# Performance work log

Hardware: AMD Instinct MI355X
Metric: run time of the kernel (lower is better)

The kernel has to match this reference:

```python
import jax, jax.numpy as jnp
import numpy as np
from jax import lax

B, D, H, W = 16, 256, 64, 64
P = 8  # patchsize
EPS = 1e-5


def setup_inputs() -> dict:
    key = jax.random.key(0)
    ks = jax.random.split(key, 8)
    s = 0.02
    return {
        "x": jax.random.normal(ks[0], (B, D, H, W), jnp.float32),
        "wq": jax.random.normal(ks[1], (D, D), jnp.float32) * s,
        "bq": jnp.zeros((D,), jnp.float32),
        "wk": jax.random.normal(ks[2], (D, D), jnp.float32) * s,
        "bk": jnp.zeros((D,), jnp.float32),
        "wv": jax.random.normal(ks[3], (D, D), jnp.float32) * s,
        "bv": jnp.zeros((D,), jnp.float32),
        "w_out": jax.random.normal(ks[4], (D, D, 3, 3), jnp.float32) * s,
        "b_out": jnp.zeros((D,), jnp.float32),
        "gamma": jnp.ones((D,), jnp.float32),
        "beta": jnp.zeros((D,), jnp.float32),
        "bn_mean": jnp.zeros((D,), jnp.float32),
        "bn_var": jnp.ones((D,), jnp.float32),
    }


def _conv1x1(x, w, b):
    # x: [b,c,h,w], w: [o,c] (1x1 conv) -> [b,o,h,w]
    return jnp.einsum('bchw,oc->bohw', x, w) + b[None, :, None, None]


def _to_patches(t, p):
    # [b,d,h,w] -> [b, p*p, d*hh*ww]  (matches view+permute(0,2,4,1,3,5)+view)
    b, d, h, w = t.shape
    hh, ww = h // p, w // p
    t = t.reshape(b, d, p, hh, p, ww).transpose(0, 2, 4, 1, 3, 5)
    return t.reshape(b, p * p, d * hh * ww)


def reference(x, wq, bq, wk, bk, wv, bv, w_out, b_out, gamma, beta, bn_mean, bn_var):
    b, d, h, w = x.shape
    p = P
    hh, ww = h // p, w // p

    q = _to_patches(_conv1x1(x, wq, bq), p)  # [b, p^2, d*hh*ww]
    k = _to_patches(_conv1x1(x, wk, bk), p)
    v = _to_patches(_conv1x1(x, wv, bv), p)

    scale = 1.0 / jnp.sqrt(jnp.asarray(q.shape[-1], q.dtype))
    scores = jnp.einsum('bqe,bke->bqk', q, k) * scale  # [b, p^2, p^2]
    attn = jax.nn.softmax(scores, axis=-1)
    out = jnp.einsum('bqk,bke->bqe', attn, v)  # [b, p^2, d*hh*ww]

    # [b,p,p,d,hh,ww] -> permute(0,3,1,4,2,5) -> [b,d,h,w]
    out = out.reshape(b, p, p, d, hh, ww).transpose(0, 3, 1, 4, 2, 5).reshape(b, d, h, w)

    # 3x3 conv, padding 1
    y = lax.conv_general_dilated(out, w_out, window_strides=(1, 1),
                                 padding=((1, 1), (1, 1)),
                                 dimension_numbers=('NCHW', 'OIHW', 'NCHW'))
    y = y + b_out[None, :, None, None]

    # BatchNorm2d (eval mode with running stats)
    inv = gamma / jnp.sqrt(bn_var + EPS)
    y = (y - bn_mean[None, :, None, None]) * inv[None, :, None, None] + beta[None, :, None, None]

    # LeakyReLU(0.2)
    return jnp.where(y >= 0, y, 0.2 * y)
```

## Files before the change

### kernel.cpp

```cpp
#include <hip/hip_runtime.h>
#include <hip/hip_bf16.h>

#define BB 16
#define SS 4096

typedef __attribute__((ext_vector_type(8))) short short8;
typedef __attribute__((ext_vector_type(4))) float float4v;

__global__ __launch_bounds__(256) void wprep_qkv(
    const float* __restrict__ wq, const float* __restrict__ wk,
    const float* __restrict__ wv, __hip_bfloat16* __restrict__ blob) {
  int chunk = blockIdx.x * 256 + threadIdx.x;
  int lane = chunk & 63;
  int ob = (chunk >> 6) & 15;
  int cb = (chunk >> 10) & 7;
  int which = chunk >> 13;
  const float* W = (which == 0) ? wq : (which == 1) ? wk : wv;
  int o = ob * 16 + (lane & 15);
  int c0 = cb * 32 + (lane >> 4) * 8;
  const float* p = W + o * 256 + c0;
  union { uint4 u; __hip_bfloat16 h[8]; } t;
#pragma unroll
  for (int j = 0; j < 8; ++j) t.h[j] = __float2bfloat16(p[j]);
  *reinterpret_cast<uint4*>(blob + (size_t)chunk * 8) = t.u;
}

__global__ __launch_bounds__(256) void qkv_mfma(
    const float* __restrict__ x, const __hip_bfloat16* __restrict__ blob,
    const float* __restrict__ bq, const float* __restrict__ bk,
    const float* __restrict__ bv,
    __hip_bfloat16* __restrict__ qb, __hip_bfloat16* __restrict__ kb,
    __hip_bfloat16* __restrict__ vb) {
  __shared__ short ls[64 * 40];
  const int which = blockIdx.z;
  const int b = blockIdx.y;
  const int s0 = blockIdx.x * 64;
  const float* bias = (which == 0) ? bq : (which == 1) ? bk : bv;
  __hip_bfloat16* outb = (which == 0) ? qb : kb;
  const int tid = threadIdx.x;
  const int wave = tid >> 6, lane = tid & 63;
  const int q = lane >> 4, m = lane & 15;
  const int sl = tid & 63;
  const int cg = tid >> 6;
  float4v acc[4][4] = {};

  for (int cb = 0; cb < 8; ++cb) {
    __syncthreads();
    {
      const float* xp = x + ((size_t)(b * 256 + cb * 32 + cg * 8)) * SS + s0 + sl;
      union { uint4 u; __hip_bfloat16 h[8]; } t;
#pragma unroll
      for (int i = 0; i < 8; ++i)
        t.h[i] = __float2bfloat16(xp[(size_t)i * SS]);
      *reinterpret_cast<uint4*>(&ls[sl * 40 + cg * 8]) = t.u;
    }
    __syncthreads();
    short8 af[4];
#pragma unroll
    for (int of = 0; of < 4; ++of)
      af[of] = *reinterpret_cast<const short8*>(
          blob +
          ((size_t)(((which * 8 + cb) * 16 + wave * 4 + of) * 64 + lane)) * 8);
    short8 xf[4];
#pragma unroll
    for (int sf = 0; sf < 4; ++sf)
      xf[sf] = *reinterpret_cast<const short8*>(&ls[(sf * 16 + m) * 40 + q * 8]);
#pragma unroll
    for (int of = 0; of < 4; ++of)
#pragma unroll
      for (int sf = 0; sf < 4; ++sf)
        acc[of][sf] = __builtin_amdgcn_mfma_f32_16x16x32_bf16(
            af[of], xf[sf], acc[of][sf], 0, 0, 0);
  }
  if (which == 2) {
    const int h = s0 >> 6;
#pragma unroll
    for (int of = 0; of < 4; ++of) {
      int o_base = wave * 64 + of * 16 + q * 4;
#pragma unroll
      for (int sf = 0; sf < 4; ++sf) {
        int w = sf * 16 + m;
        union { uint2 u; __hip_bfloat16 hh[4]; } t;
#pragma unroll
        for (int r = 0; r < 4; ++r)
          t.hh[r] = __float2bfloat16(acc[of][sf][r] + bias[o_base + r]);
        *reinterpret_cast<uint2*>(
            vb + ((size_t)((b * 64 + h) * 64 + w)) * 256 + o_base) = t.u;
      }
    }
  } else {
#pragma unroll
    for (int of = 0; of < 4; ++of) {
      int o_base = wave * 64 + of * 16 + q * 4;
#pragma unroll
      for (int r = 0; r < 4; ++r) {
        int o = o_base + r;
        float bi = bias[o];
        __hip_bfloat16* op = outb + ((size_t)(b * 256 + o)) * SS + s0 + m;
#pragma unroll
        for (int sf = 0; sf < 4; ++sf)
          op[sf * 16] = __float2bfloat16(acc[of][sf][r] + bi);
      }
    }
  }
}

__global__ __launch_bounds__(256) void scores_mfma(
    const __hip_bfloat16* __restrict__ qb, const __hip_bfloat16* __restrict__ kb,
    float* __restrict__ part) {
  const int b = blockIdx.y;
  const int d0 = blockIdx.x * 16;
  const int tid = threadIdx.x;
  const int wave = tid >> 6, lane = tid & 63;
  const int q = lane >> 4, m = lane & 15;
  const int t = wave * 16 + m;
  const int arow = (t >> 3) * 8;
  const int acol = (t & 7) * 8;
  float4v acc[4] = {};

  for (int dd = 0; dd < 16; ++dd) {
    const int d = d0 + dd;
    const __hip_bfloat16* qp = qb + ((size_t)(b * 256 + d)) * SS;
    const __hip_bfloat16* kp = kb + ((size_t)(b * 256 + d)) * SS;
#pragma unroll
    for (int khalf = 0; khalf < 2; ++khalf) {
      const int oh = khalf * 4 + q;
      short8 af = *reinterpret_cast<const short8*>(
          qp + (arow + oh) * 64 + acol);
      short8 bf[4];
#pragma unroll
      for (int nt = 0; nt < 4; ++nt) {
        int tp = nt * 16 + m;
        bf[nt] = *reinterpret_cast<const short8*>(
            kp + ((tp >> 3) * 8 + oh) * 64 + (tp & 7) * 8);
      }
#pragma unroll
      for (int nt = 0; nt < 4; ++nt)
        acc[nt] = __builtin_amdgcn_mfma_f32_16x16x32_bf16(af, bf[nt], acc[nt],
                                                          0, 0, 0);
    }
  }
  float* pp = part + ((size_t)(blockIdx.x * BB + b)) * 4096;
#pragma unroll
  for (int nt = 0; nt < 4; ++nt)
#pragma unroll
    for (int r = 0; r < 4; ++r)
      pp[(wave * 16 + q * 4 + r) * 64 + nt * 16 + m] = acc[nt][r];
}

__global__ __launch_bounds__(64) void softmax_kernel(
    const float* __restrict__ part, __hip_bfloat16* __restrict__ attnb) {
  const int t = blockIdx.x;
  const int b = blockIdx.y;
  const int lane = threadIdx.x;
  float v = 0.f;
#pragma unroll
  for (int sl = 0; sl < 16; ++sl)
    v += part[((size_t)(sl * BB + b)) * 4096 + t * 64 + lane];
  v *= 0.0078125f;
  float m = v;
#pragma unroll
  for (int off = 32; off >= 1; off >>= 1) m = fmaxf(m, __shfl_xor(m, off));
  float e = __expf(v - m);
  float s = e;
#pragma unroll
  for (int off = 32; off >= 1; off >>= 1) s += __shfl_xor(s, off);
  attnb[(b * 64 + t) * 64 + lane] = __float2bfloat16(e / s);
}

__global__ __launch_bounds__(256) void apply_mfma(
    const __hip_bfloat16* __restrict__ attnb, const __hip_bfloat16* __restrict__ vb,
    __hip_bfloat16* __restrict__ zb) {
  __shared__ short Vs[64][268];
  const int off = blockIdx.x;
  const int b = blockIdx.y;
  const int oh = off >> 3, ow = off & 7;
  const int tid = threadIdx.x;
#pragma unroll
  for (int i = 0; i < 8; ++i) {
    int chunk = i * 256 + tid;
    int tp = chunk >> 5;
    int cg = chunk & 31;
    int hh = (tp >> 3) * 8 + oh;
    int wwp = (tp & 7) * 8 + ow;
    uint4 val = *reinterpret_cast<const uint4*>(
        vb + ((size_t)((b * 64 + hh) * 64 + wwp)) * 256 + cg * 8);
    *reinterpret_cast<uint4*>(&Vs[tp][cg * 8]) = val;
  }
  __syncthreads();
  const int wave = tid >> 6, lane = tid & 63;
  const int q = lane >> 4, m = lane & 15;
  float4v acc[4][4] = {};
#pragma unroll
  for (int ks = 0; ks < 2; ++ks) {
    short8 af[4];
#pragma unroll
    for (int mt = 0; mt < 4; ++mt)
      af[mt] = *reinterpret_cast<const short8*>(
          attnb + (b * 64 + mt * 16 + m) * 64 + ks * 32 + q * 8);
    short8 bf[4];
#pragma unroll
    for (int nt = 0; nt < 4; ++nt) {
      int d = wave * 64 + nt * 16 + m;
      union { short8 v; short s[8]; } t;
#pragma unroll
      for (int j = 0; j < 8; ++j) t.s[j] = Vs[ks * 32 + q * 8 + j][d];
      bf[nt] = t.v;
    }
#pragma unroll
    for (int mt = 0; mt < 4; ++mt)
#pragma unroll
      for (int nt = 0; nt < 4; ++nt)
        acc[mt][nt] = __builtin_amdgcn_mfma_f32_16x16x32_bf16(
            af[mt], bf[nt], acc[mt][nt], 0, 0, 0);
  }
#pragma unroll
  for (int mt = 0; mt < 4; ++mt)
#pragma unroll
    for (int r = 0; r < 4; ++r) {
      int t = mt * 16 + q * 4 + r;
      int h = (t >> 3) * 8 + oh;
      int w = (t & 7) * 8 + ow;
      __hip_bfloat16* base = zb + ((size_t)((b * 64 + h) * 64 + w)) * 256;
#pragma unroll
      for (int nt = 0; nt < 4; ++nt)
        base[wave * 64 + nt * 16 + m] = __float2bfloat16(acc[mt][nt][r]);
    }
}

__global__ __launch_bounds__(256) void wprep(
    const float* __restrict__ wo, __hip_bfloat16* __restrict__ blob) {
  int chunk = blockIdx.x * 256 + threadIdx.x;
  int l = chunk & 63;
  int ob = (chunk >> 6) & 15;
  int cb = (chunk >> 10) & 7;
  int tap = chunk >> 13;
  int o = ob * 16 + (l & 15);
  int c0 = cb * 32 + (l >> 4) * 8;
  union { uint4 u; __hip_bfloat16 h[8]; } t;
#pragma unroll
  for (int j = 0; j < 8; ++j)
    t.h[j] = __float2bfloat16(wo[((size_t)(o * 256 + c0 + j)) * 9 + tap]);
  *reinterpret_cast<uint4*>(blob + (size_t)chunk * 8) = t.u;
}

__global__ __launch_bounds__(256) void conv_mfma(
    const __hip_bfloat16* __restrict__ z, const __hip_bfloat16* __restrict__ blob,
    const float* __restrict__ bo, const float* __restrict__ gm,
    const float* __restrict__ bt, const float* __restrict__ mn,
    const float* __restrict__ vr, float* __restrict__ out) {
  __shared__ short zs[2][3 * 66 * 42];
  const int idx0 = blockIdx.x;
  const int h = (idx0 & 7) * 8 + ((idx0 >> 3) & 7);
  const int b = idx0 >> 6;
  const int tid = threadIdx.x;
  const int wave = tid >> 6, lane = tid & 63;
  const int q = lane >> 4, m = lane & 15;
  float4v acc[4][4] = {};

  int s_r[4], s_wp[4], s_cg[4];
  bool s_ok[4];
  const __hip_bfloat16* s_base[4];
#pragma unroll
  for (int k = 0; k < 4; ++k) {
    int idx = tid + k * 256;
    bool act = idx < 792;
    int cg = idx & 3;
    int t2 = idx >> 2;
    int wpos = act ? (t2 % 66) : 0;
    int r = act ? (t2 / 66) : 0;
    int h_in = h - 1 + r;
    int w_in = wpos - 1;
    bool ok = act && h_in >= 0 && h_in < 64 && w_in >= 0 && w_in < 64;
    s_r[k] = r; s_wp[k] = wpos; s_cg[k] = cg; s_ok[k] = ok && act;
    s_ok[k] = ok;
    s_base[k] = z + ((size_t)((b * 64 + h_in) * 64 + w_in)) * 256 + cg * 8;
    if (!act) s_ok[k] = false;
    if (idx >= 792) { s_r[k] = 0; s_wp[k] = 0; s_cg[k] = 0; }
  }
  bool s_act[4];
#pragma unroll
  for (int k = 0; k < 4; ++k) s_act[k] = (tid + k * 256) < 792;

  uint4 pf[4];
#pragma unroll
  for (int k = 0; k < 4; ++k)
    pf[k] = s_ok[k] ? *reinterpret_cast<const uint4*>(s_base[k])
                    : make_uint4(0u, 0u, 0u, 0u);
#pragma unroll
  for (int k = 0; k < 4; ++k)
    if (s_act[k])
      *reinterpret_cast<uint4*>(
          &zs[0][(s_r[k] * 66 + s_wp[k]) * 42 + s_cg[k] * 8]) = pf[k];
  __syncthreads();

  for (int cb = 0; cb < 8; ++cb) {
    const short* cur = zs[cb & 1];
    short* nxt = zs[(cb + 1) & 1];
    if (cb < 7) {
#pragma unroll
      for (int k = 0; k < 4; ++k)
        pf[k] = s_ok[k] ? *reinterpret_cast<const uint4*>(
                              s_base[k] + (size_t)(cb + 1) * 32)
                        : make_uint4(0u, 0u, 0u, 0u);
    }
    for (int tap = 0; tap < 9; ++tap) {
      const int kh = tap / 3, kw = tap % 3;
      short8 wf[4];
#pragma unroll
      for (int of = 0; of < 4; ++of) {
        int ob = wave * 4 + of;
        wf[of] = *reinterpret_cast<const short8*>(
            blob + ((size_t)(((tap * 8 + cb) * 16 + ob) * 64 + lane)) * 8);
      }
      short8 zf[4];
#pragma unroll
      for (int wfi = 0; wfi < 4; ++wfi) {
        int wpos = wfi * 16 + m + kw;
        zf[wfi] = *reinterpret_cast<const short8*>(
            &cur[(kh * 66 + wpos) * 42 + q * 8]);
      }
#pragma unroll
      for (int of = 0; of < 4; ++of)
#pragma unroll
        for (int wfi = 0; wfi < 4; ++wfi)
          acc[of][wfi] = __builtin_amdgcn_mfma_f32_16x16x32_bf16(
              wf[of], zf[wfi], acc[of][wfi], 0, 0, 0);
    }
    if (cb < 7) {
#pragma unroll
      for (int k = 0; k < 4; ++k)
        if (s_act[k])
          *reinterpret_cast<uint4*>(
              &nxt[(s_r[k] * 66 + s_wp[k]) * 42 + s_cg[k] * 8]) = pf[k];
    }
    __syncthreads();
  }
#pragma unroll
  for (int of = 0; of < 4; ++of) {
    int o_base = wave * 64 + of * 16 + q * 4;
#pragma unroll
    for (int r = 0; r < 4; ++r) {
      int o = o_base + r;
      float sc = gm[o] * rsqrtf(vr[o] + 1e-5f);
      float sh = bt[o] + (bo[o] - mn[o]) * sc;
#pragma unroll
      for (int wfi = 0; wfi < 4; ++wfi) {
        float y = acc[of][wfi][r] * sc + sh;
        y = (y >= 0.f) ? y : 0.2f * y;
        out[(((size_t)(b * 256 + o)) * 64 + h) * 64 + wfi * 16 + m] = y;
      }
    }
  }
}

extern "C" void kernel_launch(void* const* d_in, const int* in_sizes, int n_in,
                              void* d_out, int out_size, void* d_ws,
                              size_t ws_size, hipStream_t stream) {
  (void)in_sizes; (void)n_in; (void)out_size; (void)ws_size;
  const float* x  = (const float*)d_in[0];
  const float* wq = (const float*)d_in[1];
  const float* bq = (const float*)d_in[2];
  const float* wk = (const float*)d_in[3];
  const float* bk = (const float*)d_in[4];
  const float* wv = (const float*)d_in[5];
  const float* bv = (const float*)d_in[6];
  const float* wo = (const float*)d_in[7];
  const float* bo = (const float*)d_in[8];
  const float* gm = (const float*)d_in[9];
  const float* bt = (const float*)d_in[10];
  const float* mn = (const float*)d_in[11];
  const float* vr = (const float*)d_in[12];
  float* out = (float*)d_out;

  char* ws = (char*)d_ws;
  __hip_bfloat16* qb = (__hip_bfloat16*)(ws);
  __hip_bfloat16* kb = (__hip_bfloat16*)(ws + 33554432);
  __hip_bfloat16* attnb = (__hip_bfloat16*)(ws + 67371008);
  __hip_bfloat16* blob = (__hip_bfloat16*)(ws + 67502080);
  __hip_bfloat16* vb = (__hip_bfloat16*)d_out;
  __hip_bfloat16* blob_a = (__hip_bfloat16*)((char*)d_out + 33554432);
  float* part = (float*)((char*)d_out + 37748736);

  wprep<<<288, 256, 0, stream>>>(wo, blob);
  wprep_qkv<<<96, 256, 0, stream>>>(wq, wk, wv, blob_a);
  qkv_mfma<<<dim3(64, BB, 3), 256, 0, stream>>>(x, blob_a, bq, bk, bv,
                                                qb, kb, vb);
  scores_mfma<<<dim3(16, BB), 256, 0, stream>>>(qb, kb, part);
  softmax_kernel<<<dim3(64, BB), 64, 0, stream>>>(part, attnb);
  apply_mfma<<<dim3(64, BB), 256, 0, stream>>>(attnb, vb, qb );
  conv_mfma<<<dim3(BB * 64), 256, 0, stream>>>(qb, blob, bo, gm, bt, mn, vr,
                                               out);
}
```

Measured before the change: 371.3 us.

## Fuse Q/K/V projections per block and prefetch conv weights in registers

The QKV projection now loads and converts the whole x tile (all 256 channels) into shared memory once per block and computes Q, K and V from it. Before, each of the three projections ran as its own grid slice and re-read x from global memory. The conv kernel double-buffers the weight fragments in registers, loading the next tap's weights while the current tap's MFMAs run. It also changes the shared-memory row pitch from 42 to 40 shorts and unrolls the tap loop. The trade-off is a larger shared-memory footprint and a third as many blocks in the QKV kernel, plus higher register pressure in conv, which may reduce occupancy and bring back LDS bank conflicts.

```diff
diff --git a/kernel.cpp b/kernel.cpp
--- a/kernel.cpp
+++ b/kernel.cpp
@@ -31,75 +31,78 @@
     const float* __restrict__ bv,
     __hip_bfloat16* __restrict__ qb, __hip_bfloat16* __restrict__ kb,
     __hip_bfloat16* __restrict__ vb) {
-  __shared__ short ls[64 * 40];
-  const int which = blockIdx.z;
+  __shared__ short ls[8][64 * 40];
   const int b = blockIdx.y;
   const int s0 = blockIdx.x * 64;
-  const float* bias = (which == 0) ? bq : (which == 1) ? bk : bv;
-  __hip_bfloat16* outb = (which == 0) ? qb : kb;
   const int tid = threadIdx.x;
   const int wave = tid >> 6, lane = tid & 63;
   const int q = lane >> 4, m = lane & 15;
   const int sl = tid & 63;
   const int cg = tid >> 6;
-  float4v acc[4][4] = {};
 
   for (int cb = 0; cb < 8; ++cb) {
-    __syncthreads();
-    {
-      const float* xp = x + ((size_t)(b * 256 + cb * 32 + cg * 8)) * SS + s0 + sl;
-      union { uint4 u; __hip_bfloat16 h[8]; } t;
-#pragma unroll
-      for (int i = 0; i < 8; ++i)
-        t.h[i] = __float2bfloat16(xp[(size_t)i * SS]);
-      *reinterpret_cast<uint4*>(&ls[sl * 40 + cg * 8]) = t.u;
-    }
-    __syncthreads();
-    short8 af[4];
-#pragma unroll
-    for (int of = 0; of < 4; ++of)
-      af[of] = *reinterpret_cast<const short8*>(
-          blob +
-          ((size_t)(((which * 8 + cb) * 16 + wave * 4 + of) * 64 + lane)) * 8);
-    short8 xf[4];
-#pragma unroll
-    for (int sf = 0; sf < 4; ++sf)
-      xf[sf] = *reinterpret_cast<const short8*>(&ls[(sf * 16 + m) * 40 + q * 8]);
-#pragma unroll
-    for (int of = 0; of < 4; ++of)
+    const float* xp = x + ((size_t)(b * 256 + cb * 32 + cg * 8)) * SS + s0 + sl;
+    union { uint4 u; __hip_bfloat16 h[8]; } t;
+#pragma unroll
+    for (int i = 0; i < 8; ++i)
+      t.h[i] = __float2bfloat16(xp[(size_t)i * SS]);
+    *reinterpret_cast<uint4*>(&ls[cb][sl * 40 + cg * 8]) = t.u;
+  }
+  __syncthreads();
+
+  for (int which = 0; which < 3; ++which) {
+    const float* bias = (which == 0) ? bq : (which == 1) ? bk : bv;
+    float4v acc[4][4] = {};
+#pragma unroll
+    for (int cb = 0; cb < 8; ++cb) {
+      short8 af[4];
+#pragma unroll
+      for (int of = 0; of < 4; ++of)
+        af[of] = *reinterpret_cast<const short8*>(
+            blob +
+            ((size_t)(((which * 8 + cb) * 16 + wave * 4 + of) * 64 + lane)) * 8);
+      short8 xf[4];
 #pragma unroll
       for (int sf = 0; sf < 4; ++sf)
-        acc[of][sf] = __builtin_amdgcn_mfma_f32_16x16x32_bf16(
-            af[of], xf[sf], acc[of][sf], 0, 0, 0);
-  }
-  if (which == 2) {
-    const int h = s0 >> 6;
-#pragma unroll
-    for (int of = 0; of < 4; ++of) {
-      int o_base = wave * 64 + of * 16 + q * 4;
-#pragma unroll
-      for (int sf = 0; sf < 4; ++sf) {
-        int w = sf * 16 + m;
-        union { uint2 u; __hip_bfloat16 hh[4]; } t;
-#pragma unroll
-        for (int r = 0; r < 4; ++r)
-          t.hh[r] = __float2bfloat16(acc[of][sf][r] + bias[o_base + r]);
-        *reinterpret_cast<uint2*>(
-            vb + ((size_t)((b * 64 + h) * 64 + w)) * 256 + o_base) = t.u;
-      }
-    }
-  } else {
-#pragma unroll
-    for (int of = 0; of < 4; ++of) {
-      int o_base = wave * 64 + of * 16 + q * 4;
-#pragma unroll
-      for (int r = 0; r < 4; ++r) {
-        int o = o_base + r;
-        float bi = bias[o];
-        __hip_bfloat16* op = outb + ((size_t)(b * 256 + o)) * SS + s0 + m;
+        xf[sf] =
+            *reinterpret_cast<const short8*>(&ls[cb][(sf * 16 + m) * 40 + q * 8]);
+#pragma unroll
+      for (int of = 0; of < 4; ++of)
 #pragma unroll
         for (int sf = 0; sf < 4; ++sf)
-          op[sf * 16] = __float2bfloat16(acc[of][sf][r] + bi);
+          acc[of][sf] = __builtin_amdgcn_mfma_f32_16x16x32_bf16(
+              af[of], xf[sf], acc[of][sf], 0, 0, 0);
+    }
+    if (which == 2) {
+      const int h = s0 >> 6;
+#pragma unroll
+      for (int of = 0; of < 4; ++of) {
+        int o_base = wave * 64 + of * 16 + q * 4;
+#pragma unroll
+        for (int sf = 0; sf < 4; ++sf) {
+          int w = sf * 16 + m;
+          union { uint2 u; __hip_bfloat16 hh[4]; } t;
+#pragma unroll
+          for (int r = 0; r < 4; ++r)
+            t.hh[r] = __float2bfloat16(acc[of][sf][r] + bias[o_base + r]);
+          *reinterpret_cast<uint2*>(
+              vb + ((size_t)((b * 64 + h) * 64 + w)) * 256 + o_base) = t.u;
+        }
+      }
+    } else {
+      __hip_bfloat16* outb = (which == 0) ? qb : kb;
+#pragma unroll
+      for (int of = 0; of < 4; ++of) {
+        int o_base = wave * 64 + of * 16 + q * 4;
+#pragma unroll
+        for (int r = 0; r < 4; ++r) {
+          int o = o_base + r;
+          float bi = bias[o];
+          __hip_bfloat16* op = outb + ((size_t)(b * 256 + o)) * SS + s0 + m;
+#pragma unroll
+          for (int sf = 0; sf < 4; ++sf)
+            op[sf * 16] = __float2bfloat16(acc[of][sf][r] + bi);
+        }
       }
     }
   }
@@ -249,7 +252,7 @@
     const float* __restrict__ bo, const float* __restrict__ gm,
     const float* __restrict__ bt, const float* __restrict__ mn,
     const float* __restrict__ vr, float* __restrict__ out) {
-  __shared__ short zs[2][3 * 66 * 42];
+  __shared__ short zs[2][3 * 66 * 40];
   const int idx0 = blockIdx.x;
   const int h = (idx0 & 7) * 8 + ((idx0 >> 3) & 7);
   const int b = idx0 >> 6;
@@ -259,7 +262,7 @@
   float4v acc[4][4] = {};
 
   int s_r[4], s_wp[4], s_cg[4];
-  bool s_ok[4];
+  bool s_ok[4], s_act[4];
   const __hip_bfloat16* s_base[4];
 #pragma unroll
   for (int k = 0; k < 4; ++k) {
@@ -272,15 +275,11 @@
     int h_in = h - 1 + r;
     int w_in = wpos - 1;
     bool ok = act && h_in >= 0 && h_in < 64 && w_in >= 0 && w_in < 64;
-    s_r[k] = r; s_wp[k] = wpos; s_cg[k] = cg; s_ok[k] = ok && act;
-    s_ok[k] = ok;
+    if (!act) { r = 0; wpos = 0; cg = 0; }
+    s_r[k] = r; s_wp[k] = wpos; s_cg[k] = cg;
+    s_ok[k] = ok; s_act[k] = act;
     s_base[k] = z + ((size_t)((b * 64 + h_in) * 64 + w_in)) * 256 + cg * 8;
-    if (!act) s_ok[k] = false;
-    if (idx >= 792) { s_r[k] = 0; s_wp[k] = 0; s_cg[k] = 0; }
-  }
-  bool s_act[4];
-#pragma unroll
-  for (int k = 0; k < 4; ++k) s_act[k] = (tid + k * 256) < 792;
+  }
 
   uint4 pf[4];
 #pragma unroll
@@ -291,9 +290,16 @@
   for (int k = 0; k < 4; ++k)
     if (s_act[k])
       *reinterpret_cast<uint4*>(
-          &zs[0][(s_r[k] * 66 + s_wp[k]) * 42 + s_cg[k] * 8]) = pf[k];
+          &zs[0][(s_r[k] * 66 + s_wp[k]) * 40 + s_cg[k] * 8]) = pf[k];
+
+  short8 wfb[2][4];
+#pragma unroll
+  for (int of = 0; of < 4; ++of)
+    wfb[0][of] = *reinterpret_cast<const short8*>(
+        blob + ((size_t)((0 * 16 + wave * 4 + of) * 64 + lane)) * 8);
   __syncthreads();
 
+#pragma unroll 2
   for (int cb = 0; cb < 8; ++cb) {
     const short* cur = zs[cb & 1];
     short* nxt = zs[(cb + 1) & 1];
@@ -304,35 +310,42 @@
                               s_base[k] + (size_t)(cb + 1) * 32)
                         : make_uint4(0u, 0u, 0u, 0u);
     }
+#pragma unroll
     for (int tap = 0; tap < 9; ++tap) {
       const int kh = tap / 3, kw = tap % 3;
-      short8 wf[4];
-#pragma unroll
-      for (int of = 0; of < 4; ++of) {
-        int ob = wave * 4 + of;
-        wf[of] = *reinterpret_cast<const short8*>(
-            blob + ((size_t)(((tap * 8 + cb) * 16 + ob) * 64 + lane)) * 8);
+      const int p = (cb + tap) & 1;
+      {
+        const int ntap = (tap == 8) ? 0 : tap + 1;
+        const int ncb = (tap == 8) ? cb + 1 : cb;
+        if (ncb < 8) {
+#pragma unroll
+          for (int of = 0; of < 4; ++of)
+            wfb[p ^ 1][of] = *reinterpret_cast<const short8*>(
+                blob +
+                ((size_t)(((ntap * 8 + ncb) * 16 + wave * 4 + of) * 64 + lane)) *
+                    8);
+        }
       }
       short8 zf[4];
 #pragma unroll
       for (int wfi = 0; wfi < 4; ++wfi) {
         int wpos = wfi * 16 + m + kw;
         zf[wfi] = *reinterpret_cast<const short8*>(
-            &cur[(kh * 66 + wpos) * 42 + q * 8]);
+            &cur[(kh * 66 + wpos) * 40 + q * 8]);
       }
 #pragma unroll
       for (int of = 0; of < 4; ++of)
 #pragma unroll
         for (int wfi = 0; wfi < 4; ++wfi)
           acc[of][wfi] = __builtin_amdgcn_mfma_f32_16x16x32_bf16(
-              wf[of], zf[wfi], acc[of][wfi], 0, 0, 0);
+              wfb[p][of], zf[wfi], acc[of][wfi], 0, 0, 0);
     }
     if (cb < 7) {
 #pragma unroll
       for (int k = 0; k < 4; ++k)
         if (s_act[k])
           *reinterpret_cast<uint4*>(
-              &nxt[(s_r[k] * 66 + s_wp[k]) * 42 + s_cg[k] * 8]) = pf[k];
+              &nxt[(s_r[k] * 66 + s_wp[k]) * 40 + s_cg[k] * 8]) = pf[k];
     }
     __syncthreads();
   }
@@ -384,8 +397,8 @@
 
   wprep<<<288, 256, 0, stream>>>(wo, blob);
   wprep_qkv<<<96, 256, 0, stream>>>(wq, wk, wv, blob_a);
-  qkv_mfma<<<dim3(64, BB, 3), 256, 0, stream>>>(x, blob_a, bq, bk, bv,
-                                                qb, kb, vb);
+  qkv_mfma<<<dim3(64, BB), 256, 0, stream>>>(x, blob_a, bq, bk, bv,
+                                             qb, kb, vb);
   scores_mfma<<<dim3(16, BB), 256, 0, stream>>>(qb, kb, part);
   softmax_kernel<<<dim3(64, BB), 64, 0, stream>>>(part, attnb);
   apply_mfma<<<dim3(64, BB), 256, 0, stream>>>(attnb, vb, qb );
```

Result: faster. 352.6 us (-5.1%).
